# Optimization experiments

Measured on AMD Instinct MI355X. Metric: run time of the kernel, lower is better.

Reference implementation:

```python
import jax, jax.numpy as jnp
import numpy as np

B, H, W, C = 8, 128, 128, 192
G, K = 6, 3
K2 = K * K
GC = C // G
OFFSET_SCALE = 0.1
DN = ('NHWC', 'HWIO', 'NHWC')


def setup_inputs() -> dict:
    key = jax.random.key(0)
    ks = jax.random.split(key, 8)
    s = 1.0 / np.sqrt(C)
    return {
        'x': jax.random.normal(ks[0], (B, H, W, C), jnp.float32),
        'w_in': jax.random.normal(ks[1], (C, C), jnp.float32) * s,
        'b_in': jnp.zeros((C,), jnp.float32),
        'w_dw': jax.random.normal(ks[2], (3, 3, 1, C), jnp.float32) / 3.0,  # depthwise 3x3, HWIO
        'b_dw': jnp.zeros((C,), jnp.float32),
        'w_pw': jax.random.normal(ks[3], (1, 1, C, C), jnp.float32) * s,  # 1x1 conv
        'b_pw': jnp.zeros((C,), jnp.float32),
        'w_off': jax.random.normal(ks[4], (C, G * K2 * 2), jnp.float32) * 0.01,
        'b_off': jnp.zeros((G * K2 * 2,), jnp.float32),
        'w_mask': jax.random.normal(ks[5], (C, G * K2), jnp.float32) * 0.01,
        'b_mask': jnp.zeros((G * K2,), jnp.float32),
        'w_out': jax.random.normal(ks[6], (C, C), jnp.float32) * s,
        'b_out': jnp.zeros((C,), jnp.float32),
    }


def _deform_forward(x, w_in, b_in, w_dw, b_dw, w_pw, b_pw, w_off, b_off, w_mask, b_mask, w_out, b_out):
    x_proj = x @ w_in + b_in  # [B,H,W,C]

    # dw_conv: depthwise 3x3 -> SiLU -> 1x1 pointwise (all channels-last)
    xd = jax.lax.conv_general_dilated(x, w_dw, (1, 1), 'SAME', dimension_numbers=DN,
                                      feature_group_count=C) + b_dw
    xd = xd * jax.nn.sigmoid(xd)  # SiLU
    xd = jax.lax.conv_general_dilated(xd, w_pw, (1, 1), 'SAME', dimension_numbers=DN) + b_pw

    offsets = (xd @ w_off + b_off).reshape(B, H, W, G, K2, 2) * OFFSET_SCALE
    attn = jax.nn.softmax((xd @ w_mask + b_mask).reshape(B, H, W, G, K2), axis=-1)
    attn = jnp.nan_to_num(attn, nan=0.0)

    r = jnp.arange(-(K // 2), K // 2 + 1, dtype=jnp.float32)
    ref_grid = jnp.stack(jnp.meshgrid(r, r, indexing='ij'), -1).reshape(K2, 2)  # [K2,2]
    pos = ref_grid + offsets  # [B,H,W,G,K2,2]
    pos_h = jnp.clip(pos[..., 0] + jnp.arange(H, dtype=jnp.float32)[None, :, None, None, None], 0.0, H - 1)
    pos_w = jnp.clip(pos[..., 1] + jnp.arange(W, dtype=jnp.float32)[None, None, :, None, None], 0.0, W - 1)

    xg = x_proj.reshape(B, H * W, G, GC)

    def gather(hi, wi):
        idx = (hi * W + wi).reshape(B, H * W, G, 1)
        return jnp.take_along_axis(xg, idx, axis=1).reshape(B, H, W, G, GC)

    def tap(acc, inputs):
        ph, pw, a = inputs  # each [B,H,W,G]
        hf = jnp.clip(ph.astype(jnp.int32), 0, H - 1)
        wf = jnp.clip(pw.astype(jnp.int32), 0, W - 1)
        hc = jnp.minimum(hf + 1, H - 1)
        wc = jnp.minimum(wf + 1, W - 1)
        hw = ph - hf.astype(jnp.float32)
        ww = pw - wf.astype(jnp.float32)
        sampled = (gather(hf, wf) * ((1 - hw) * (1 - ww))[..., None]
                   + gather(hf, wc) * ((1 - hw) * ww)[..., None]
                   + gather(hc, wf) * (hw * (1 - ww))[..., None]
                   + gather(hc, wc) * (hw * ww)[..., None])
        return acc + sampled * a[..., None], None

    xs = (jnp.moveaxis(pos_h, -1, 0), jnp.moveaxis(pos_w, -1, 0), jnp.moveaxis(attn, -1, 0))
    out, _ = jax.lax.scan(tap, jnp.zeros((B, H, W, G, GC), x.dtype), xs)
    return out.reshape(B, H, W, C) @ w_out + b_out


def reference(x, w_in, b_in, w_dw, b_dw, w_pw, b_pw, w_off, b_off, w_mask, b_mask, w_out, b_out):
    return _deform_forward(x, w_in, b_in, w_dw, b_dw, w_pw, b_pw,
                           w_off, b_off, w_mask, b_mask, w_out, b_out)
```

## Files before the change

### kernel.cpp

```cpp
#include <hip/hip_runtime.h>
#include <hip/hip_bf16.h>

#define Bn 8
#define Hn 128
#define Wn 128
#define Cn 192
#define Gn 6
#define GCn 32
#define NPIX (Bn*Hn*Wn)

typedef __attribute__((ext_vector_type(8))) short v8s;
typedef __attribute__((ext_vector_type(4))) float v4f;
typedef __attribute__((ext_vector_type(2))) float v2f;
typedef __hip_bfloat16 bf16;

__device__ __forceinline__ float b2f(bf16 v){ return __bfloat162float(v); }
__device__ __forceinline__ float lo16(unsigned u){ return __uint_as_float(u << 16); }
__device__ __forceinline__ float hi16(unsigned u){ return __uint_as_float(u & 0xffff0000u); }
__device__ __forceinline__ v2f up2(unsigned u){
    return (v2f){ __uint_as_float(u << 16), __uint_as_float(u & 0xffff0000u) };
}

__global__ __launch_bounds__(256) void cvt_bf16(const float* __restrict__ in,
                                                bf16* __restrict__ out, long n)
{
    long base = ((long)blockIdx.x*256 + threadIdx.x)*8;
    if (base >= n) return;
    float v[8];
    *(float4*)(v)   = *(const float4*)(in + base);
    *(float4*)(v+4) = *(const float4*)(in + base + 4);
    bf16 o[8];
    #pragma unroll
    for (int j=0;j<8;j++) o[j] = __float2bfloat16(v[j]);
    *(uint4*)(out + base) = *(uint4*)o;
}

__global__ __launch_bounds__(256) void swizzle_w(const float* __restrict__ w,
                                                 bf16* __restrict__ out, int N)
{
    int idx = blockIdx.x*256 + threadIdx.x;
    int j = idx & 7, lane = (idx>>3)&63, ks = (idx>>9)%6, nt = idx/3072;
    int k = ks*32 + ((lane>>4)<<3) + j;
    int n = (nt<<4) + (lane&15);
    out[idx] = (n < N) ? __float2bfloat16(w[k*N + n]) : __float2bfloat16(0.0f);
}

__global__ __launch_bounds__(256) void swizzle_omc(const float* __restrict__ wpw,
        const float* __restrict__ woff, const float* __restrict__ wmask,
        const float* __restrict__ bpw, const float* __restrict__ boff,
        const float* __restrict__ bmask, bf16* __restrict__ out, float* __restrict__ biascat)
{
    int idx = blockIdx.x*256 + threadIdx.x;
    int j = idx & 7, lane = (idx>>3)&63, ks = (idx>>9)%6, nt = idx/3072;
    int k = ks*32 + ((lane>>4)<<3) + j;
    int m = (nt<<4) + (lane&15);
    float acc = 0.0f;
    if (m < 162) {
        const float* wrow = wpw + k*192;
        for (int n=0; n<192; n++) {
            float wc = (m < 108) ? woff[n*108 + m] : wmask[n*54 + (m-108)];
            acc += wrow[n] * wc;
        }
    }
    out[idx] = __float2bfloat16(acc);
    if (idx < 192) {
        float bv = 0.0f;
        if (idx < 162) {
            bv = (idx < 108) ? boff[idx] : bmask[idx-108];
            for (int n=0; n<192; n++) {
                float wc = (idx < 108) ? woff[n*108 + idx] : wmask[n*54 + (idx-108)];
                bv += bpw[n] * wc;
            }
        }
        biascat[idx] = bv;
    }
}

__device__ __forceinline__ void store_out(bf16* p, float v){ *p = __float2bfloat16(v); }
__device__ __forceinline__ void store_out(float* p, float v){ *p = v; }

template<typename OutT>
__global__ __launch_bounds__(256, 2) void gemm6r(const bf16* __restrict__ A,
        const v8s* __restrict__ wfrag, const float* __restrict__ bias,
        OutT* __restrict__ Cmat, int Nreal, int Nstride)
{
    int tid = threadIdx.x;
    int wave = tid >> 6, lane = tid & 63;
    int q = lane >> 4, r = lane & 15;
    int n = blockIdx.x;
    int l = (n & 7) * 128 + (n >> 3);
    int yhalf = l & 1;
    int mt0 = l >> 1;
    const v8s* wsrc = wfrag + yhalf*(36*64) + lane;
    v8s breg[36];
    #pragma unroll
    for (int f=0; f<36; f++) breg[f] = wsrc[f*64];
    int col0 = yhalf*96;
    float bv[6];
    #pragma unroll
    for (int nt=0; nt<6; nt++) {
        int col = col0 + nt*16 + r;
        bv[nt] = (col < Nreal) ? bias[col] : 0.0f;
    }
    const int MT = NPIX/64;
    for (int mt = mt0; mt < MT; mt += 512) {
        const bf16* Ap = A + (size_t)(mt*64 + wave*16 + r)*Cn + q*8;
        v8s av[6];
        #pragma unroll
        for (int ks=0; ks<6; ks++) av[ks] = *(const v8s*)(Ap + ks*32);
        v4f acc[6];
        #pragma unroll
        for (int nt=0;nt<6;nt++) acc[nt] = (v4f){0.f,0.f,0.f,0.f};
        #pragma unroll
        for (int ks=0; ks<6; ks++)
            #pragma unroll
            for (int nt=0;nt<6;nt++)
                acc[nt] = __builtin_amdgcn_mfma_f32_16x16x32_bf16(
                              av[ks], breg[nt*6+ks], acc[nt], 0, 0, 0);
        int orow = mt*64 + wave*16 + q*4;
        #pragma unroll
        for (int nt=0;nt<6;nt++) {
            int col = col0 + nt*16 + r;
            if (col < Nreal) {
                #pragma unroll
                for (int i=0;i<4;i++)
                    store_out(&Cmat[(size_t)(orow+i)*Nstride + col], acc[nt][i] + bv[nt]);
            }
        }
    }
}

__global__ __launch_bounds__(256, 4) void dw_silu(const bf16* __restrict__ x,
        const bf16* __restrict__ wdwb, const float* __restrict__ bdw, bf16* __restrict__ out)
{
    int bid = blockIdx.x;
    int bsw = (bid & 7) * 768 + (bid >> 3);
    int idx = bsw*256 + threadIdx.x;
    int c16 = idx % 12; int pix = idx / 12;
    int b = pix >> 14; int hw = pix & 16383; int h = hw >> 7, w = hw & 127;
    int cb = c16*16;
    v2f acc2[8];
    #pragma unroll
    for (int j=0;j<8;j++) acc2[j] = (v2f){bdw[cb+2*j], bdw[cb+2*j+1]};
    #pragma unroll
    for (int dy=-1;dy<=1;dy++){
        int hh=h+dy; if ((unsigned)hh >= (unsigned)Hn) continue;
        #pragma unroll
        for (int dx=-1;dx<=1;dx++){
            int ww=w+dx; if ((unsigned)ww >= (unsigned)Wn) continue;
            const uint4* xp = (const uint4*)(x + ((size_t)((b<<14)+(hh<<7)+ww))*Cn + cb);
            const uint4* wp = (const uint4*)(wdwb + ((dy+1)*3+(dx+1))*Cn + cb);
            #pragma unroll
            for (int cs=0;cs<2;cs++){
                uint4 xu = xp[cs], wu = wp[cs];
                unsigned xa[4] = {xu.x,xu.y,xu.z,xu.w};
                unsigned wa[4] = {wu.x,wu.y,wu.z,wu.w};
                #pragma unroll
                for (int t=0;t<4;t++)
                    acc2[cs*4+t] += up2(xa[t]) * up2(wa[t]);
            }
        }
    }
    bf16 ov[16];
    #pragma unroll
    for (int j=0;j<8;j++){
        float v0 = acc2[j].x, v1 = acc2[j].y;
        ov[2*j]   = __float2bfloat16(v0 / (1.f + __expf(-v0)));
        ov[2*j+1] = __float2bfloat16(v1 / (1.f + __expf(-v1)));
    }
    uint4* op = (uint4*)(out + (size_t)pix*Cn + cb);
    op[0] = ((uint4*)ov)[0];
    op[1] = ((uint4*)ov)[1];
}


#define LOADTAP(K, S)                                                        \
  { float ph = (float)(h + (K)/3 - 1) + 0.1f*lo16(op[K]);                    \
    float pw = (float)(w + (K)%3 - 1) + 0.1f*hi16(op[K]);                    \
    ph = fminf(fmaxf(ph, 0.f), 127.f);                                       \
    pw = fminf(fmaxf(pw, 0.f), 127.f);                                       \
    int hf = (int)ph, wf = (int)pw;                                          \
    fh##S = ph - (float)hf; fw##S = pw - (float)wf;                          \
    int hc = min(hf+1,127), wc = min(wf+1,127);                              \
    const uint4* p00 = (const uint4*)(xb + ((hf<<7)+wf)*Cn);                 \
    const uint4* p01 = (const uint4*)(xb + ((hf<<7)+wc)*Cn);                 \
    const uint4* p10 = (const uint4*)(xb + ((hc<<7)+wf)*Cn);                 \
    const uint4* p11 = (const uint4*)(xb + ((hc<<7)+wc)*Cn);                 \
    S##00[0]=p00[0]; S##00[1]=p00[1]; S##01[0]=p01[0]; S##01[1]=p01[1];      \
    S##10[0]=p10[0]; S##10[1]=p10[1]; S##11[0]=p11[0]; S##11[1]=p11[1]; }

#define ACCTAP(K, S)                                                         \
  { float a = att[K];                                                        \
    float w00=(1.f-fh##S)*(1.f-fw##S)*a, w01=(1.f-fh##S)*fw##S*a,            \
          w10=fh##S*(1.f-fw##S)*a, w11=fh##S*fw##S*a;                        \
    _Pragma("unroll")                                                        \
    for (int cs=0;cs<2;cs++){                                                \
      unsigned u00[4]={S##00[cs].x,S##00[cs].y,S##00[cs].z,S##00[cs].w};     \
      unsigned u01[4]={S##01[cs].x,S##01[cs].y,S##01[cs].z,S##01[cs].w};     \
      unsigned u10[4]={S##10[cs].x,S##10[cs].y,S##10[cs].z,S##10[cs].w};     \
      unsigned u11[4]={S##11[cs].x,S##11[cs].y,S##11[cs].z,S##11[cs].w};     \
      _Pragma("unroll")                                                      \
      for (int t=0;t<4;t++)                                                  \
        acc2[cs*4+t] += up2(u00[t])*w00 + up2(u01[t])*w01                    \
                      + up2(u10[t])*w10 + up2(u11[t])*w11; } }

__global__ __launch_bounds__(256, 4) void deform_sample(const bf16* __restrict__ P,
        const bf16* __restrict__ OM, bf16* __restrict__ S)
{
    int bid = blockIdx.x;
    int bsw = (bid & 7) * 768 + (bid >> 3);
    int idx = bsw*256 + threadIdx.x;
    int half = idx & 1;
    int g = (idx >> 1) % 6;
    int pix = idx / 12;
    int b = pix >> 14; int hw = pix & 16383; int h = hw >> 7, w = hw & 127;
    const bf16* om = OM + (size_t)pix*162;
    const bf16* oml = om + 108 + g*9;
    const unsigned* ofp = (const unsigned*)(om + g*18);

    unsigned op[9];
    #pragma unroll
    for (int k=0;k<9;k++) op[k] = ofp[k];

    float att[9];
    float m = -1e30f;
    #pragma unroll
    for (int k=0;k<9;k++){ att[k] = b2f(oml[k]); m = fmaxf(m, att[k]); }
    float ssum = 0.f;
    #pragma unroll
    for (int k=0;k<9;k++){ att[k] = __expf(att[k]-m); ssum += att[k]; }
    float inv = 1.f/ssum;
    #pragma unroll
    for (int k=0;k<9;k++) att[k] *= inv;

    int chbase = g*GCn + half*16;
    const bf16* xb = P + ((((size_t)b) << 14))*Cn + chbase;

    v2f acc2[8];
    #pragma unroll
    for (int j=0;j<8;j++) acc2[j] = (v2f){0.f, 0.f};

    uint4 A00[2],A01[2],A10[2],A11[2]; float fhA,fwA;
    uint4 B00[2],B01[2],B10[2],B11[2]; float fhB,fwB;

    LOADTAP(0, A)
    LOADTAP(1, B)
    ACCTAP(0, A)  LOADTAP(2, A)
    ACCTAP(1, B)  LOADTAP(3, B)
    ACCTAP(2, A)  LOADTAP(4, A)
    ACCTAP(3, B)  LOADTAP(5, B)
    ACCTAP(4, A)  LOADTAP(6, A)
    ACCTAP(5, B)  LOADTAP(7, B)
    ACCTAP(6, A)  LOADTAP(8, A)
    ACCTAP(7, B)
    ACCTAP(8, A)

    bf16 ov[16];
    #pragma unroll
    for (int j=0;j<8;j++){
        ov[2*j]   = __float2bfloat16(acc2[j].x);
        ov[2*j+1] = __float2bfloat16(acc2[j].y);
    }
    uint4* sp = (uint4*)(S + (size_t)pix*Cn + chbase);
    sp[0] = ((uint4*)ov)[0];
    sp[1] = ((uint4*)ov)[1];
}

extern "C" void kernel_launch(void* const* d_in, const int* in_sizes, int n_in,
                              void* d_out, int out_size, void* d_ws, size_t ws_size,
                              hipStream_t stream)
{
    const float* x      = (const float*)d_in[0];
    const float* w_in   = (const float*)d_in[1];
    const float* b_in   = (const float*)d_in[2];
    const float* w_dw   = (const float*)d_in[3];
    const float* b_dw   = (const float*)d_in[4];
    const float* w_pw   = (const float*)d_in[5];
    const float* b_pw   = (const float*)d_in[6];
    const float* w_off  = (const float*)d_in[7];
    const float* b_off  = (const float*)d_in[8];
    const float* w_mask = (const float*)d_in[9];
    const float* b_mask = (const float*)d_in[10];
    const float* w_out  = (const float*)d_in[11];
    const float* b_out  = (const float*)d_in[12];
    float* out = (float*)d_out;

    char* ws = (char*)d_ws;
    size_t off = 0;
    auto carve = [&](size_t bytes)->char* {
        char* p = ws + off; off += (bytes + 255) & ~(size_t)255; return p; };
    bf16* XB  = (bf16*)carve((size_t)NPIX*Cn*2);
    bf16* P   = (bf16*)carve((size_t)NPIX*Cn*2);
    bf16* D   = (bf16*)carve((size_t)NPIX*Cn*2);
    bf16* OM  = (bf16*)carve((size_t)NPIX*162*2);
    bf16* wfI = (bf16*)carve(36864*2);
    bf16* wfO = (bf16*)carve(36864*2);
    bf16* wfM = (bf16*)carve(36864*2);
    float* bM = (float*)carve(192*4);
    bf16* WDW = (bf16*)carve(1728*2);

    dim3 blk(256);
    cvt_bf16<<<12288, blk, 0, stream>>>(x, XB, (long)NPIX*Cn);
    cvt_bf16<<<1,     blk, 0, stream>>>(w_dw, WDW, 1728);
    swizzle_w<<<144, blk, 0, stream>>>(w_in,  wfI, 192);
    swizzle_w<<<144, blk, 0, stream>>>(w_out, wfO, 192);
    swizzle_omc<<<144, blk, 0, stream>>>(w_pw, w_off, w_mask, b_pw, b_off, b_mask, wfM, bM);

    gemm6r<bf16><<<1024, blk, 0, stream>>>(XB, (const v8s*)wfI, b_in, P, 192, 192);

    dw_silu<<<6144, blk, 0, stream>>>(XB, WDW, b_dw, D);

    gemm6r<bf16><<<1024, blk, 0, stream>>>(D, (const v8s*)wfM, bM, OM, 162, 162);

    deform_sample<<<6144, blk, 0, stream>>>(P, OM, D);

    gemm6r<float><<<1024, blk, 0, stream>>>(D, (const v8s*)wfO, b_out, out, 192, 192);
}
```

Measured before the change: 418.5 us.

## Split weight-fold dot products across 8 lanes and preload interior dw taps

The fused pointwise·offset/mask weight-folding kernel now splits each 192-length dot product across 8 lanes of 24 elements each and combines them with xor shuffles. It launches 8x more threads, so this tiny serial setup kernel gets more parallelism. The depthwise conv gains an interior fast path that issues all 9 tap loads before doing the math, which raises memory-level parallelism. Launch bounds drop to 2 waves per SIMD so the extra registers fit, at some cost in occupancy.

Measured after the change: 399.5 us. 4.6% less time.

```diff
diff --git a/kernel.cpp b/kernel.cpp
--- a/kernel.cpp
+++ b/kernel.cpp
@@ -50,29 +50,49 @@
         const float* __restrict__ bpw, const float* __restrict__ boff,
         const float* __restrict__ bmask, bf16* __restrict__ out, float* __restrict__ biascat)
 {
-    int idx = blockIdx.x*256 + threadIdx.x;
-    int j = idx & 7, lane = (idx>>3)&63, ks = (idx>>9)%6, nt = idx/3072;
-    int k = ks*32 + ((lane>>4)<<3) + j;
-    int m = (nt<<4) + (lane&15);
-    float acc = 0.0f;
-    if (m < 162) {
-        const float* wrow = wpw + k*192;
-        for (int n=0; n<192; n++) {
-            float wc = (m < 108) ? woff[n*108 + m] : wmask[n*54 + (m-108)];
-            acc += wrow[n] * wc;
-        }
-    }
-    out[idx] = __float2bfloat16(acc);
-    if (idx < 192) {
+    int gid = blockIdx.x*256 + threadIdx.x;
+    int s = gid & 7; int n0 = s*24;
+    if (gid < 36864*8) {
+        int idx = gid >> 3;
+        int j = idx & 7, lane = (idx>>3)&63, ks = (idx>>9)%6, nt = idx/3072;
+        int k = ks*32 + ((lane>>4)<<3) + j;
+        int m = (nt<<4) + (lane&15);
+        float acc = 0.0f;
+        if (m < 108) {
+            const float* wr = wpw + k*192 + n0;
+            const float* wc = woff + (size_t)n0*108 + m;
+            #pragma unroll 6
+            for (int i=0;i<24;i++) acc += wr[i] * wc[(size_t)i*108];
+        } else if (m < 162) {
+            const float* wr = wpw + k*192 + n0;
+            const float* wc = wmask + (size_t)n0*54 + (m-108);
+            #pragma unroll 6
+            for (int i=0;i<24;i++) acc += wr[i] * wc[(size_t)i*54];
+        }
+        acc += __shfl_xor(acc, 1);
+        acc += __shfl_xor(acc, 2);
+        acc += __shfl_xor(acc, 4);
+        if (s == 0) out[idx] = __float2bfloat16(acc);
+    } else {
+        int t = gid - 36864*8;
+        int idx = t >> 3;
         float bv = 0.0f;
-        if (idx < 162) {
-            bv = (idx < 108) ? boff[idx] : bmask[idx-108];
-            for (int n=0; n<192; n++) {
-                float wc = (idx < 108) ? woff[n*108 + idx] : wmask[n*54 + (idx-108)];
-                bv += bpw[n] * wc;
-            }
-        }
-        biascat[idx] = bv;
+        if (idx < 108) {
+            #pragma unroll 6
+            for (int i=0;i<24;i++) bv += bpw[n0+i] * woff[(size_t)(n0+i)*108 + idx];
+        } else if (idx < 162) {
+            #pragma unroll 6
+            for (int i=0;i<24;i++) bv += bpw[n0+i] * wmask[(size_t)(n0+i)*54 + (idx-108)];
+        }
+        bv += __shfl_xor(bv, 1);
+        bv += __shfl_xor(bv, 2);
+        bv += __shfl_xor(bv, 4);
+        if (s == 0) {
+            float base = 0.0f;
+            if (idx < 108) base = boff[idx];
+            else if (idx < 162) base = bmask[idx-108];
+            biascat[idx] = bv + base;
+        }
     }
 }
 
@@ -130,7 +150,7 @@
     }
 }
 
-__global__ __launch_bounds__(256, 4) void dw_silu(const bf16* __restrict__ x,
+__global__ __launch_bounds__(256, 2) void dw_silu(const bf16* __restrict__ x,
         const bf16* __restrict__ wdwb, const float* __restrict__ bdw, bf16* __restrict__ out)
 {
     int bid = blockIdx.x;
@@ -142,22 +162,47 @@
     v2f acc2[8];
     #pragma unroll
     for (int j=0;j<8;j++) acc2[j] = (v2f){bdw[cb+2*j], bdw[cb+2*j+1]};
-    #pragma unroll
-    for (int dy=-1;dy<=1;dy++){
-        int hh=h+dy; if ((unsigned)hh >= (unsigned)Hn) continue;
-        #pragma unroll
-        for (int dx=-1;dx<=1;dx++){
-            int ww=w+dx; if ((unsigned)ww >= (unsigned)Wn) continue;
-            const uint4* xp = (const uint4*)(x + ((size_t)((b<<14)+(hh<<7)+ww))*Cn + cb);
-            const uint4* wp = (const uint4*)(wdwb + ((dy+1)*3+(dx+1))*Cn + cb);
+
+    const bf16* xc = x + (size_t)pix*Cn + cb;
+    if (h > 0 && h < 127 && w > 0 && w < 127) {
+        uint4 xd[9][2], wd[9][2];
+        #pragma unroll
+        for (int t9=0;t9<9;t9++){
+            const int dy = t9/3 - 1, dx = t9%3 - 1;
+            const uint4* xp = (const uint4*)(xc + (dy*Wn + dx)*Cn);
+            const uint4* wp = (const uint4*)(wdwb + t9*Cn + cb);
+            xd[t9][0]=xp[0]; xd[t9][1]=xp[1];
+            wd[t9][0]=wp[0]; wd[t9][1]=wp[1];
+        }
+        #pragma unroll
+        for (int t9=0;t9<9;t9++){
             #pragma unroll
             for (int cs=0;cs<2;cs++){
-                uint4 xu = xp[cs], wu = wp[cs];
-                unsigned xa[4] = {xu.x,xu.y,xu.z,xu.w};
-                unsigned wa[4] = {wu.x,wu.y,wu.z,wu.w};
+                unsigned xa[4]={xd[t9][cs].x,xd[t9][cs].y,xd[t9][cs].z,xd[t9][cs].w};
+                unsigned wa[4]={wd[t9][cs].x,wd[t9][cs].y,wd[t9][cs].z,wd[t9][cs].w};
                 #pragma unroll
                 for (int t=0;t<4;t++)
                     acc2[cs*4+t] += up2(xa[t]) * up2(wa[t]);
+            }
+        }
+    } else {
+        #pragma unroll
+        for (int dy=-1;dy<=1;dy++){
+            int hh=h+dy; if ((unsigned)hh >= (unsigned)Hn) continue;
+            #pragma unroll
+            for (int dx=-1;dx<=1;dx++){
+                int ww=w+dx; if ((unsigned)ww >= (unsigned)Wn) continue;
+                const uint4* xp = (const uint4*)(x + ((size_t)((b<<14)+(hh<<7)+ww))*Cn + cb);
+                const uint4* wp = (const uint4*)(wdwb + ((dy+1)*3+(dx+1))*Cn + cb);
+                #pragma unroll
+                for (int cs=0;cs<2;cs++){
+                    uint4 xu = xp[cs], wu = wp[cs];
+                    unsigned xa[4] = {xu.x,xu.y,xu.z,xu.w};
+                    unsigned wa[4] = {wu.x,wu.y,wu.z,wu.w};
+                    #pragma unroll
+                    for (int t=0;t<4;t++)
+                        acc2[cs*4+t] += up2(xa[t]) * up2(wa[t]);
+                }
             }
         }
     }
@@ -304,7 +349,7 @@
     cvt_bf16<<<1,     blk, 0, stream>>>(w_dw, WDW, 1728);
     swizzle_w<<<144, blk, 0, stream>>>(w_in,  wfI, 192);
     swizzle_w<<<144, blk, 0, stream>>>(w_out, wfO, 192);
-    swizzle_omc<<<144, blk, 0, stream>>>(w_pw, w_off, w_mask, b_pw, b_off, b_mask, wfM, bM);
+    swizzle_omc<<<1158, blk, 0, stream>>>(w_pw, w_off, w_mask, b_pw, b_off, b_mask, wfM, bM);
 
     gemm6r<bf16><<<1024, blk, 0, stream>>>(XB, (const v8s*)wfI, b_in, P, 192, 192);
 
```
